# Performance work log

Hardware: AMD Instinct MI355X
Metric: run time of the kernel (lower is better)

The kernel has to match this reference:

```python
import jax, jax.numpy as jnp
import numpy as np
import math

BLUR, P, SCALING = 0.05, 2.0, 0.9
DIAMETER = 8.0  # static bound on max |x-y| for unit-normal 1-D data (geomloss derives it from data)
NEG = -1e9     # masked log-weight


def _eps_schedule():
    # geomloss epsilon_schedule: diameter^p -> blur^p, geometric with ratio scaling^p
    eps = [DIAMETER ** P]
    eps += list(np.exp(np.arange(P * math.log(DIAMETER), P * math.log(BLUR), P * math.log(SCALING))))
    eps += [BLUR ** P]
    return np.asarray(eps, dtype=np.float32)


def _softmin(eps, C, h):
    # h: [m] = log-weights + dual/eps ; returns [n] = -eps*logsumexp_j(h_j - C_ij/eps)
    return -eps * jax.nn.logsumexp(h[None, :] - C / eps, axis=1)


def _sinkhorn_divergence(x, y, logw):
    # x, y: [B] 1-D point clouds for one output dim; logw: [B] masked log-weights.
    # Debiased Sinkhorn divergence S = OT_eps(a,b) - 0.5 OT(a,a) - 0.5 OT(b,b), p=2 cost |x-y|^2/2.
    Cxy = 0.5 * (x[:, None] - y[None, :]) ** 2
    Cxx = 0.5 * (x[:, None] - x[None, :]) ** 2
    Cyy = 0.5 * (y[:, None] - y[None, :]) ** 2
    eps_list = jnp.asarray(_eps_schedule())
    e0 = eps_list[0]
    f = _softmin(e0, Cxy, logw)    # dual on x for OT(a,b)
    g = _softmin(e0, Cxy.T, logw)  # dual on y for OT(a,b)
    a = _softmin(e0, Cxx, logw)    # self dual on x
    b = _softmin(e0, Cyy, logw)    # self dual on y

    def step(carry, eps):
        f, g, a, b = carry
        ft = _softmin(eps, Cxy, logw + g / eps)
        gt = _softmin(eps, Cxy.T, logw + f / eps)
        at = _softmin(eps, Cxx, logw + a / eps)
        bt = _softmin(eps, Cyy, logw + b / eps)
        return (0.5 * (f + ft), 0.5 * (g + gt), 0.5 * (a + at), 0.5 * (b + bt)), None

    (f, g, a, b), _ = jax.lax.scan(step, (f, g, a, b), eps_list)
    # last extrapolation at final eps (full updates, no damping)
    e = eps_list[-1]
    f, g = _softmin(e, Cxy, logw + g / e), _softmin(e, Cxy.T, logw + f / e)
    a = 0.5 * (a + _softmin(e, Cxx, logw + a / e))
    b = 0.5 * (b + _softmin(e, Cyy, logw + b / e))
    w = jnp.exp(logw)  # 1/n on valid samples, 0 on masked
    return jnp.sum(w * (f - a)) + jnp.sum(w * (g - b))


def reference(predictions, targets):
    # predictions, targets: [B, D]; NaNs in targets mark invalid samples per dim
    mask = ~jnp.isnan(targets)                      # [B, D]
    y = jnp.where(mask, targets, 0.0)
    counts = jnp.sum(mask, axis=0)                  # [D]
    logn = jnp.log(jnp.maximum(counts, 1).astype(predictions.dtype))
    logw = jnp.where(mask, -logn[None, :], NEG)     # [B, D]
    per_dim = jax.vmap(_sinkhorn_divergence, in_axes=(1, 1, 1))(predictions, y, logw)
    per_dim = jnp.where(counts > 1, per_dim, 0.0)   # dims with <=1 valid sample -> 0
    total = jnp.mean(per_dim)                       # weights=None -> mean over dims
    return total, per_dim


def setup_inputs() -> dict:
    key = jax.random.key(0)
    k1, k2, k3 = jax.random.split(key, 3)
    B, D = 2048, 8
    preds = jax.random.normal(k1, (B, D), dtype=jnp.float32)
    targ = jax.random.normal(k2, (B, D), dtype=jnp.float32)
    nan_mask = jax.random.uniform(k3, (B, D)) < 0.1
    targ = jnp.where(nan_mask, jnp.nan, targ)
    return {"predictions": preds, "targets": targ}
```

## Files before the change

### kernel.cpp

```cpp
#include <hip/hip_runtime.h>
#include <math.h>

#define BN 2048
#define DN 8
#define NEGW -1e9f
#define TPB 256
#define RPB 64
#define RS 16
#define JSPLIT 16
#define SLOTS (BN/2)
#define SPC (SLOTS/JSPLIT)
#define CPAD 65

typedef float f2 __attribute__((ext_vector_type(2)));

static __device__ __forceinline__ float wave_reduce_sum(float v){
  #pragma unroll
  for (int off = 32; off > 0; off >>= 1) v += __shfl_xor(v, off, 64);
  return v;
}

__global__ void setup_kernel(const float* __restrict__ pred, const float* __restrict__ targ,
                             float* __restrict__ xcol, float* __restrict__ ycol,
                             float* __restrict__ logw, float* __restrict__ counts){
  int d = blockIdx.x;
  int t = threadIdx.x;
  int lane = t & 63, wave = t >> 6;
  float mk[BN/256];
  float c = 0.f;
  for (int k = 0; k < BN/256; k++){
    int i = t + k*256;
    float tv = targ[i*DN + d];
    bool m = !(tv != tv);
    mk[k] = m ? 1.f : 0.f;
    c += mk[k];
    ycol[d*BN + i] = m ? tv : 0.f;
    xcol[d*BN + i] = pred[i*DN + d];
  }
  __shared__ float sh[4];
  __shared__ float logn_sh;
  float cw = wave_reduce_sum(c);
  if (lane == 0) sh[wave] = cw;
  __syncthreads();
  if (t == 0){
    float tot = sh[0] + sh[1] + sh[2] + sh[3];
    counts[d] = tot;
    logn_sh = logf(fmaxf(tot, 1.f));
  }
  __syncthreads();
  float ln = logn_sh;
  for (int k = 0; k < BN/256; k++){
    int i = t + k*256;
    logw[d*BN + i] = (mk[k] > 0.f) ? -ln : NEGW;
  }
}

__global__ __launch_bounds__(TPB) void sink_step(
      const float* __restrict__ xcol, const float* __restrict__ ycol,
      const float* __restrict__ logw,
      const float* __restrict__ dold, float* __restrict__ dnew,
      float eps, float inv_eps, int mode){
  const float L2E = 1.44269504088896340736f;
  const float LN2 = 0.69314718055994530942f;
  __shared__ float4 pair4[JSPLIT*CPAD];
  __shared__ float2 pms[JSPLIT][RPB];

  int bid = blockIdx.x;
  int rc  = bid & 31;
  int mat = (bid >> 5) & 3;
  int d   = bid >> 7;
  int t   = threadIdx.x;
  int rs  = t & (RS-1);
  int jc  = t >> 4;

  const float* xb = xcol + d*BN;
  const float* yb = ycol + d*BN;
  const float* lw = logw + d*BN;
  const float* ri; const float* pj; int hsel;
  switch (mat){
    case 0:  ri = xb; pj = yb; hsel = 1; break;
    case 1:  ri = yb; pj = xb; hsel = 0; break;
    case 2:  ri = xb; pj = xb; hsel = 2; break;
    default: ri = yb; pj = yb; hsel = 3; break;
  }
  const float* hd  = dold + (size_t)hsel*DN*BN + d*BN;
  const float* dmp = dold + (size_t)mat *DN*BN + d*BN;
  float*       op  = dnew + (size_t)mat *DN*BN + d*BN;

  const float c1 = L2E * inv_eps;
  const float c2 = 0.5f * inv_eps * L2E;

  const float2* pj2 = (const float2*)pj;
  const float2* lw2 = (const float2*)lw;
  const float2* hd2 = (const float2*)hd;
  #pragma unroll
  for (int k = 0; k < SLOTS/TPB; k++){
    int idx = t + k*TPB;
    int phys = idx + (idx >> 6);
    float2 y2 = pj2[idx];
    float2 l2 = lw2[idx];
    float h0 = l2.x, h1 = l2.y;
    if (mode != 0){
      float2 dd = hd2[idx];
      h0 = fmaf(dd.x, inv_eps, h0);
      h1 = fmaf(dd.y, inv_eps, h1);
    }
    pair4[phys] = make_float4(y2.x, y2.y,
                              fmaf(-c2*y2.x, y2.x, L2E*h0),
                              fmaf(-c2*y2.y, y2.y, L2E*h1));
  }

  int row0 = rc*RPB + rs;
  f2 a2[4];
  #pragma unroll
  for (int r = 0; r < 4; r++){
    float xi = ri[row0 + RS*r];
    float al = c1 * xi;
    a2[r] = (f2){al, al};
  }
  __syncthreads();

  const float4* cb = pair4 + jc*CPAD;
  float mrow[4];
  f2 sA[4], sB[4];
  #pragma unroll
  for (int r = 0; r < 4; r++){
    mrow[r] = -INFINITY;
    sA[r] = (f2){0.f, 0.f};
    sB[r] = (f2){0.f, 0.f};
  }
  #pragma unroll 1
  for (int q = 0; q < SPC; q += 8){
    float4 P0 = cb[q+0]; float4 P1 = cb[q+1];
    float4 P2 = cb[q+2]; float4 P3 = cb[q+3];
    float4 P4 = cb[q+4]; float4 P5 = cb[q+5];
    float4 P6 = cb[q+6]; float4 P7 = cb[q+7];
    #pragma unroll
    for (int r = 0; r < 4; r++){
      f2 a = a2[r];
      f2 v0 = __builtin_elementwise_fma(a, (f2){P0.x,P0.y}, (f2){P0.z,P0.w});
      f2 v1 = __builtin_elementwise_fma(a, (f2){P1.x,P1.y}, (f2){P1.z,P1.w});
      f2 v2 = __builtin_elementwise_fma(a, (f2){P2.x,P2.y}, (f2){P2.z,P2.w});
      f2 v3 = __builtin_elementwise_fma(a, (f2){P3.x,P3.y}, (f2){P3.z,P3.w});
      f2 v4 = __builtin_elementwise_fma(a, (f2){P4.x,P4.y}, (f2){P4.z,P4.w});
      f2 v5 = __builtin_elementwise_fma(a, (f2){P5.x,P5.y}, (f2){P5.z,P5.w});
      f2 v6 = __builtin_elementwise_fma(a, (f2){P6.x,P6.y}, (f2){P6.z,P6.w});
      f2 v7 = __builtin_elementwise_fma(a, (f2){P7.x,P7.y}, (f2){P7.z,P7.w});
      f2 t0 = __builtin_elementwise_max(v0, v1);
      f2 t1 = __builtin_elementwise_max(v2, v3);
      f2 t2 = __builtin_elementwise_max(v4, v5);
      f2 t3 = __builtin_elementwise_max(v6, v7);
      f2 u0 = __builtin_elementwise_max(t0, t1);
      f2 u1 = __builtin_elementwise_max(t2, t3);
      f2 w  = __builtin_elementwise_max(u0, u1);
      float bm = fmaxf(w.x, w.y);
      float mo = mrow[r];
      float mn = fmaxf(mo, bm);
      float sc = __builtin_amdgcn_exp2f(mo - mn);
      mrow[r] = mn;
      f2 scv = (f2){sc, sc};
      f2 mv  = (f2){mn, mn};
      f2 e;
      e = v0 - mv;
      f2 x0 = (f2){__builtin_amdgcn_exp2f(e.x), __builtin_amdgcn_exp2f(e.y)};
      e = v1 - mv;
      f2 x1 = (f2){__builtin_amdgcn_exp2f(e.x), __builtin_amdgcn_exp2f(e.y)};
      e = v2 - mv;
      f2 x2 = (f2){__builtin_amdgcn_exp2f(e.x), __builtin_amdgcn_exp2f(e.y)};
      e = v3 - mv;
      f2 x3 = (f2){__builtin_amdgcn_exp2f(e.x), __builtin_amdgcn_exp2f(e.y)};
      e = v4 - mv;
      f2 x4 = (f2){__builtin_amdgcn_exp2f(e.x), __builtin_amdgcn_exp2f(e.y)};
      e = v5 - mv;
      f2 x5 = (f2){__builtin_amdgcn_exp2f(e.x), __builtin_amdgcn_exp2f(e.y)};
      e = v6 - mv;
      f2 x6 = (f2){__builtin_amdgcn_exp2f(e.x), __builtin_amdgcn_exp2f(e.y)};
      e = v7 - mv;
      f2 x7 = (f2){__builtin_amdgcn_exp2f(e.x), __builtin_amdgcn_exp2f(e.y)};
      sA[r] = __builtin_elementwise_fma(sA[r], scv, x0);
      sB[r] = __builtin_elementwise_fma(sB[r], scv, x1);
      sA[r] += x2;  sB[r] += x3;
      sA[r] += x4;  sB[r] += x5;
      sA[r] += x6;  sB[r] += x7;
    }
  }
  #pragma unroll
  for (int r = 0; r < 4; r++){
    f2 s = sA[r] + sB[r];
    pms[jc][rs + RS*r] = make_float2(mrow[r], s.x + s.y);
  }
  __syncthreads();

  if (t < RPB){
    int row = rc*RPB + t;
    float M = -INFINITY;
    #pragma unroll
    for (int k = 0; k < JSPLIT; k++) M = fmaxf(M, pms[k][t].x);
    float s = 0.f;
    #pragma unroll
    for (int k = 0; k < JSPLIT; k++){
      float2 p = pms[k][t];
      s = fmaf(p.y, __builtin_amdgcn_exp2f(p.x - M), s);
    }
    float xi = ri[row];
    float beta = c2 * xi * xi;
    float lse2 = (M + __builtin_amdgcn_logf(s)) - beta;
    float tn = -eps * (LN2 * lse2);
    float outv;
    if (mode == 1 || (mode == 2 && mat >= 2)) outv = 0.5f * (dmp[row] + tn);
    else                                      outv = tn;
    op[row] = outv;
  }
}

__global__ void reduce_kernel(const float* __restrict__ dual, const float* __restrict__ logw,
                              const float* __restrict__ counts, float* __restrict__ out){
  int d = blockIdx.x;
  int t = threadIdx.x;
  int lane = t & 63, wave = t >> 6;
  float acc = 0.f;
  for (int k = 0; k < BN/256; k++){
    int i = t + k*256;
    float w  = expf(logw[d*BN + i]);
    float fv = dual[0*DN*BN + d*BN + i];
    float gv = dual[1*DN*BN + d*BN + i];
    float av = dual[2*DN*BN + d*BN + i];
    float bv = dual[3*DN*BN + d*BN + i];
    acc += w * ((fv - av) + (gv - bv));
  }
  __shared__ float sh[4];
  float aw = wave_reduce_sum(acc);
  if (lane == 0) sh[wave] = aw;
  __syncthreads();
  if (t == 0){
    float tot = sh[0] + sh[1] + sh[2] + sh[3];
    out[1 + d] = (counts[d] > 1.5f) ? tot : 0.f;
  }
}

__global__ void total_kernel(float* __restrict__ out){
  if (threadIdx.x == 0 && blockIdx.x == 0){
    float s = 0.f;
    for (int d = 0; d < DN; d++) s += out[1 + d];
    out[0] = s / (float)DN;
  }
}

extern "C" void kernel_launch(void* const* d_in, const int* in_sizes, int n_in,
                              void* d_out, int out_size, void* d_ws, size_t ws_size,
                              hipStream_t stream){
  const float* pred = (const float*)d_in[0];
  const float* targ = (const float*)d_in[1];
  float* out = (float*)d_out;
  float* ws  = (float*)d_ws;

  float* xcol   = ws;
  float* ycol   = ws + (size_t)DN*BN;
  float* logw   = ws + (size_t)2*DN*BN;
  float* counts = ws + (size_t)3*DN*BN;
  float* buf0   = ws + (size_t)3*DN*BN + 64;
  float* buf1   = buf0 + (size_t)4*DN*BN;

  float eps_list[64]; int n = 0;
  {
    const double P = 2.0, DIAM = 8.0, BLUR = 0.05, SC = 0.9;
    double ls = P*log(DIAM), le = P*log(BLUR), st = P*log(SC);
    eps_list[n++] = (float)pow(DIAM, P);
    int cnt = (int)ceil((le - ls)/st);
    for (int k = 0; k < cnt; k++) eps_list[n++] = (float)exp(ls + st*(double)k);
    eps_list[n++] = (float)(BLUR*BLUR);
  }

  setup_kernel<<<DN, 256, 0, stream>>>(pred, targ, xcol, ycol, logw, counts);

  dim3 grid(DN*4*32), blk(TPB);
  float* cur = buf0; float* nxt = buf1;
  {
    float e = eps_list[0];
    sink_step<<<grid, blk, 0, stream>>>(xcol, ycol, logw, cur, cur, e, 1.f/e, 0);
  }
  for (int k = 0; k < n; k++){
    float e = eps_list[k];
    sink_step<<<grid, blk, 0, stream>>>(xcol, ycol, logw, cur, nxt, e, 1.f/e, 1);
    float* tmp = cur; cur = nxt; nxt = tmp;
  }
  {
    float e = eps_list[n-1];
    sink_step<<<grid, blk, 0, stream>>>(xcol, ycol, logw, cur, nxt, e, 1.f/e, 2);
    float* tmp = cur; cur = nxt; nxt = tmp;
  }
  reduce_kernel<<<DN, 256, 0, stream>>>(cur, logw, counts, out);
  total_kernel<<<1, 64, 0, stream>>>(out);
}
```

Baseline: 1.075 ms.

## Double rows per block and precompute next-step log-weight potentials in epilogue

Each block now handles 128 rows instead of 64, so the staged column tile in shared memory is reused across twice as many rows, and the grid shrinks to 512 blocks. The epilogue also writes h = logw + dual/eps_next into a separate buffer. The next step can then load h directly instead of loading both logw and the dual and doing an fma. The cost is more registers per thread (8 row accumulators), fewer blocks to fill the GPU, and an extra global write per row.

```diff
diff --git a/kernel.cpp b/kernel.cpp
--- a/kernel.cpp
+++ b/kernel.cpp
@@ -5,7 +5,7 @@
 #define DN 8
 #define NEGW -1e9f
 #define TPB 256
-#define RPB 64
+#define RPB 128
 #define RS 16
 #define JSPLIT 16
 #define SLOTS (BN/2)
@@ -18,6 +18,9 @@
   #pragma unroll
   for (int off = 32; off > 0; off >>= 1) v += __shfl_xor(v, off, 64);
   return v;
+}
+static __device__ __forceinline__ f2 exp2_hw(f2 e){
+  return (f2){__builtin_amdgcn_exp2f(e.x), __builtin_amdgcn_exp2f(e.y)};
 }
 
 __global__ void setup_kernel(const float* __restrict__ pred, const float* __restrict__ targ,
@@ -59,16 +62,17 @@
       const float* __restrict__ xcol, const float* __restrict__ ycol,
       const float* __restrict__ logw,
       const float* __restrict__ dold, float* __restrict__ dnew,
-      float eps, float inv_eps, int mode){
+      const float* __restrict__ Hold, float* __restrict__ Hnew,
+      float eps, float inv_eps, float inv_eps_next, int mode){
   const float L2E = 1.44269504088896340736f;
   const float LN2 = 0.69314718055994530942f;
   __shared__ float4 pair4[JSPLIT*CPAD];
   __shared__ float2 pms[JSPLIT][RPB];
 
   int bid = blockIdx.x;
-  int rc  = bid & 31;
-  int mat = (bid >> 5) & 3;
-  int d   = bid >> 7;
+  int rc  = bid & 15;
+  int mat = (bid >> 4) & 3;
+  int d   = bid >> 6;
   int t   = threadIdx.x;
   int rs  = t & (RS-1);
   int jc  = t >> 4;
@@ -83,37 +87,31 @@
     case 2:  ri = xb; pj = xb; hsel = 2; break;
     default: ri = yb; pj = yb; hsel = 3; break;
   }
-  const float* hd  = dold + (size_t)hsel*DN*BN + d*BN;
+  const float* hp  = Hold + (size_t)hsel*DN*BN + d*BN;
   const float* dmp = dold + (size_t)mat *DN*BN + d*BN;
   float*       op  = dnew + (size_t)mat *DN*BN + d*BN;
+  float*       oh  = Hnew + (size_t)mat *DN*BN + d*BN;
 
   const float c1 = L2E * inv_eps;
   const float c2 = 0.5f * inv_eps * L2E;
 
   const float2* pj2 = (const float2*)pj;
-  const float2* lw2 = (const float2*)lw;
-  const float2* hd2 = (const float2*)hd;
+  const float2* h2src = (mode == 0) ? (const float2*)lw : (const float2*)hp;
   #pragma unroll
   for (int k = 0; k < SLOTS/TPB; k++){
     int idx = t + k*TPB;
     int phys = idx + (idx >> 6);
     float2 y2 = pj2[idx];
-    float2 l2 = lw2[idx];
-    float h0 = l2.x, h1 = l2.y;
-    if (mode != 0){
-      float2 dd = hd2[idx];
-      h0 = fmaf(dd.x, inv_eps, h0);
-      h1 = fmaf(dd.y, inv_eps, h1);
-    }
+    float2 hh = h2src[idx];
     pair4[phys] = make_float4(y2.x, y2.y,
-                              fmaf(-c2*y2.x, y2.x, L2E*h0),
-                              fmaf(-c2*y2.y, y2.y, L2E*h1));
+                              fmaf(-c2*y2.x, y2.x, L2E*hh.x),
+                              fmaf(-c2*y2.y, y2.y, L2E*hh.y));
   }
 
   int row0 = rc*RPB + rs;
-  f2 a2[4];
-  #pragma unroll
-  for (int r = 0; r < 4; r++){
+  f2 a2[8];
+  #pragma unroll
+  for (int r = 0; r < 8; r++){
     float xi = ri[row0 + RS*r];
     float al = c1 * xi;
     a2[r] = (f2){al, al};
@@ -121,10 +119,10 @@
   __syncthreads();
 
   const float4* cb = pair4 + jc*CPAD;
-  float mrow[4];
-  f2 sA[4], sB[4];
-  #pragma unroll
-  for (int r = 0; r < 4; r++){
+  float mrow[8];
+  f2 sA[8], sB[8];
+  #pragma unroll
+  for (int r = 0; r < 8; r++){
     mrow[r] = -INFINITY;
     sA[r] = (f2){0.f, 0.f};
     sB[r] = (f2){0.f, 0.f};
@@ -136,7 +134,7 @@
     float4 P4 = cb[q+4]; float4 P5 = cb[q+5];
     float4 P6 = cb[q+6]; float4 P7 = cb[q+7];
     #pragma unroll
-    for (int r = 0; r < 4; r++){
+    for (int r = 0; r < 8; r++){
       f2 a = a2[r];
       f2 v0 = __builtin_elementwise_fma(a, (f2){P0.x,P0.y}, (f2){P0.z,P0.w});
       f2 v1 = __builtin_elementwise_fma(a, (f2){P1.x,P1.y}, (f2){P1.z,P1.w});
@@ -160,23 +158,14 @@
       mrow[r] = mn;
       f2 scv = (f2){sc, sc};
       f2 mv  = (f2){mn, mn};
-      f2 e;
-      e = v0 - mv;
-      f2 x0 = (f2){__builtin_amdgcn_exp2f(e.x), __builtin_amdgcn_exp2f(e.y)};
-      e = v1 - mv;
-      f2 x1 = (f2){__builtin_amdgcn_exp2f(e.x), __builtin_amdgcn_exp2f(e.y)};
-      e = v2 - mv;
-      f2 x2 = (f2){__builtin_amdgcn_exp2f(e.x), __builtin_amdgcn_exp2f(e.y)};
-      e = v3 - mv;
-      f2 x3 = (f2){__builtin_amdgcn_exp2f(e.x), __builtin_amdgcn_exp2f(e.y)};
-      e = v4 - mv;
-      f2 x4 = (f2){__builtin_amdgcn_exp2f(e.x), __builtin_amdgcn_exp2f(e.y)};
-      e = v5 - mv;
-      f2 x5 = (f2){__builtin_amdgcn_exp2f(e.x), __builtin_amdgcn_exp2f(e.y)};
-      e = v6 - mv;
-      f2 x6 = (f2){__builtin_amdgcn_exp2f(e.x), __builtin_amdgcn_exp2f(e.y)};
-      e = v7 - mv;
-      f2 x7 = (f2){__builtin_amdgcn_exp2f(e.x), __builtin_amdgcn_exp2f(e.y)};
+      f2 x0 = exp2_hw(v0 - mv);
+      f2 x1 = exp2_hw(v1 - mv);
+      f2 x2 = exp2_hw(v2 - mv);
+      f2 x3 = exp2_hw(v3 - mv);
+      f2 x4 = exp2_hw(v4 - mv);
+      f2 x5 = exp2_hw(v5 - mv);
+      f2 x6 = exp2_hw(v6 - mv);
+      f2 x7 = exp2_hw(v7 - mv);
       sA[r] = __builtin_elementwise_fma(sA[r], scv, x0);
       sB[r] = __builtin_elementwise_fma(sB[r], scv, x1);
       sA[r] += x2;  sB[r] += x3;
@@ -185,7 +174,7 @@
     }
   }
   #pragma unroll
-  for (int r = 0; r < 4; r++){
+  for (int r = 0; r < 8; r++){
     f2 s = sA[r] + sB[r];
     pms[jc][rs + RS*r] = make_float2(mrow[r], s.x + s.y);
   }
@@ -210,6 +199,7 @@
     if (mode == 1 || (mode == 2 && mat >= 2)) outv = 0.5f * (dmp[row] + tn);
     else                                      outv = tn;
     op[row] = outv;
+    oh[row] = fmaf(outv, inv_eps_next, lw[row]);
   }
 }
 
@@ -260,6 +250,8 @@
   float* counts = ws + (size_t)3*DN*BN;
   float* buf0   = ws + (size_t)3*DN*BN + 64;
   float* buf1   = buf0 + (size_t)4*DN*BN;
+  float* H0     = buf1 + (size_t)4*DN*BN;
+  float* H1     = H0   + (size_t)4*DN*BN;
 
   float eps_list[64]; int n = 0;
   {
@@ -273,21 +265,28 @@
 
   setup_kernel<<<DN, 256, 0, stream>>>(pred, targ, xcol, ycol, logw, counts);
 
-  dim3 grid(DN*4*32), blk(TPB);
-  float* cur = buf0; float* nxt = buf1;
+  dim3 grid(DN*4*16), blk(TPB);
+  float* cur = buf0;  float* nxt = buf1;
+  float* Hc  = H0;    float* Hn  = H1;
   {
     float e = eps_list[0];
-    sink_step<<<grid, blk, 0, stream>>>(xcol, ycol, logw, cur, cur, e, 1.f/e, 0);
+    sink_step<<<grid, blk, 0, stream>>>(xcol, ycol, logw, cur, cur, Hc, Hc,
+                                        e, 1.f/e, 1.f/eps_list[0], 0);
   }
   for (int k = 0; k < n; k++){
     float e = eps_list[k];
-    sink_step<<<grid, blk, 0, stream>>>(xcol, ycol, logw, cur, nxt, e, 1.f/e, 1);
-    float* tmp = cur; cur = nxt; nxt = tmp;
+    float en = (k+1 < n) ? eps_list[k+1] : eps_list[n-1];
+    sink_step<<<grid, blk, 0, stream>>>(xcol, ycol, logw, cur, nxt, Hc, Hn,
+                                        e, 1.f/e, 1.f/en, 1);
+    float* tb = cur; cur = nxt; nxt = tb;
+    float* th = Hc;  Hc  = Hn;  Hn  = th;
   }
   {
     float e = eps_list[n-1];
-    sink_step<<<grid, blk, 0, stream>>>(xcol, ycol, logw, cur, nxt, e, 1.f/e, 2);
-    float* tmp = cur; cur = nxt; nxt = tmp;
+    sink_step<<<grid, blk, 0, stream>>>(xcol, ycol, logw, cur, nxt, Hc, Hn,
+                                        e, 1.f/e, 1.f/e, 2);
+    float* tb = cur; cur = nxt; nxt = tb;
+    float* th = Hc;  Hc  = Hn;  Hn  = th;
   }
   reduce_kernel<<<DN, 256, 0, stream>>>(cur, logw, counts, out);
   total_kernel<<<1, 64, 0, stream>>>(out);
```

Result: faster. 1.042 ms, median of 2 (-3.1%).
